# Performance work log

Measured on AMD Instinct MI355X. Metric: run time of the kernel, lower is better.

The kernel has to match this reference:

```python
import jax, jax.numpy as jnp
import numpy as np

DEPTH, DIM, HEADS = 12, 768, 12
B, N = 2, 2048
HEAD_DIM = DIM // HEADS


def setup_inputs() -> dict:
    key = jax.random.key(0)
    ks = jax.random.split(key, 8)
    s = 0.02
    return {
        "x": jax.random.normal(ks[0], (B, N, DIM), jnp.float32),
        "sequence_ids": jnp.sort(jax.random.randint(ks[1], (B, N), 0, 8), axis=-1),
        "sequence_mask": jnp.zeros((B, N), dtype=bool),
        "ln1_w": jnp.ones((DEPTH, DIM), jnp.float32),
        "ln1_b": jnp.zeros((DEPTH, DIM), jnp.float32),
        "qkv_w": jax.random.normal(ks[2], (DEPTH, DIM, 3 * DIM), jnp.float32) * s,
        "qkv_b": jnp.zeros((DEPTH, 3 * DIM), jnp.float32),
        "proj_w": jax.random.normal(ks[3], (DEPTH, DIM, DIM), jnp.float32) * s,
        "proj_b": jnp.zeros((DEPTH, DIM), jnp.float32),
        "ls1_g": jnp.full((DEPTH, DIM), 1e-5, jnp.float32),
        "ln2_w": jnp.ones((DEPTH, DIM), jnp.float32),
        "ln2_b": jnp.zeros((DEPTH, DIM), jnp.float32),
        "fc1_w": jax.random.normal(ks[4], (DEPTH, DIM, 4 * DIM), jnp.float32) * s,
        "fc1_b": jnp.zeros((DEPTH, 4 * DIM), jnp.float32),
        "fc2_w": jax.random.normal(ks[5], (DEPTH, 4 * DIM, DIM), jnp.float32) * s,
        "fc2_b": jnp.zeros((DEPTH, DIM), jnp.float32),
        "ls2_g": jnp.full((DEPTH, DIM), 1e-5, jnp.float32),
        "r": 0,
    }


def _layernorm(x, w, b, eps=1e-5):
    m = x.mean(-1, keepdims=True)
    v = ((x - m) ** 2).mean(-1, keepdims=True)
    return (x - m) * jax.lax.rsqrt(v + eps) * w + b


def _attention(x, attn_mask, qkv_w, qkv_b, proj_w, proj_b):
    b, n, c = x.shape
    qkv = (x @ qkv_w + qkv_b).reshape(b, n, 3, HEADS, HEAD_DIM)
    qkv = jnp.transpose(qkv, (2, 0, 3, 1, 4))  # [3, B, H, N, hd]
    q, k, v = qkv[0], qkv[1], qkv[2]
    attn = jnp.einsum("bhqd,bhkd->bhqk", q, k) * (HEAD_DIM ** -0.5)
    neg_inf = jnp.finfo(attn.dtype).min
    attn = jnp.where(attn_mask[:, None, :, :], neg_inf, attn)  # broadcast over heads
    attn = jax.nn.softmax(attn, axis=-1)
    out = jnp.einsum("bhqk,bhkd->bhqd", attn, v)
    out = jnp.transpose(out, (0, 2, 1, 3)).reshape(b, n, c)
    return out @ proj_w + proj_b


def reference(x, sequence_ids, sequence_mask, ln1_w, ln1_b, qkv_w, qkv_b,
              proj_w, proj_b, ls1_g, ln2_w, ln2_b, fc1_w, fc1_b,
              fc2_w, fc2_b, ls2_g, r):
    # attn_mask: True where attention is NOT allowed
    attn_mask = sequence_ids[:, :, None] != sequence_ids[:, None, :]
    attn_mask = attn_mask | sequence_mask[:, :, None] | sequence_mask[:, None, :]
    for i in range(DEPTH):
        h = _layernorm(x, ln1_w[i], ln1_b[i])
        h = _attention(h, attn_mask, qkv_w[i], qkv_b[i], proj_w[i], proj_b[i])
        x = x + h * ls1_g[i]
        h = _layernorm(x, ln2_w[i], ln2_b[i])
        h = jax.nn.gelu(h @ fc1_w[i] + fc1_b[i], approximate=False) @ fc2_w[i] + fc2_b[i]
        x = x + h * ls2_g[i]
    return x
```

## Files before the change

### kernel.cpp

```cpp
#include <hip/hip_runtime.h>

#define NDEPTH 12
#define NDIM 768
#define NHEADS 12
#define NB 2
#define NSEQ 2048
#define MTOK (NB*NSEQ)

typedef short bf16x8 __attribute__((ext_vector_type(8)));
typedef float f32x4 __attribute__((ext_vector_type(4)));
typedef unsigned short u16;
typedef unsigned int u32;

#define L2E 1.44269504088896f

__device__ inline u16 f2bf(float f){
  union { float f; u32 u; } x; x.f = f;
  u32 r = x.u + 0x7fffu + ((x.u >> 16) & 1u);
  return (u16)(r >> 16);
}

__device__ inline f32x4 mfma16(bf16x8 a, bf16x8 b, f32x4 c){
  return __builtin_amdgcn_mfma_f32_16x16x32_bf16(a, b, c, 0, 0, 0);
}

#define GLOAD_LDS(gsrc, ldst) __builtin_amdgcn_global_load_lds( \
    (const __attribute__((address_space(1))) u32*)(gsrc), \
    (__attribute__((address_space(3))) u32*)(ldst), 16, 0, 0)

__device__ inline void ln_body(const float* __restrict__ x,
    const float* __restrict__ w, const float* __restrict__ b,
    u16* __restrict__ out, int blk){
  int wv = threadIdx.x >> 6, lane = threadIdx.x & 63;
  int row = blk * 4 + wv;
  const float* xr = x + (size_t)row * NDIM;
  float v[12];
  #pragma unroll
  for (int j = 0; j < 12; j++) v[j] = xr[lane + 64*j];
  float s = 0.f;
  #pragma unroll
  for (int j = 0; j < 12; j++) s += v[j];
  #pragma unroll
  for (int m = 1; m < 64; m <<= 1) s += __shfl_xor(s, m);
  float mean = s * (1.0f/768.0f);
  float q = 0.f;
  #pragma unroll
  for (int j = 0; j < 12; j++){ float d = v[j]-mean; q += d*d; }
  #pragma unroll
  for (int m = 1; m < 64; m <<= 1) q += __shfl_xor(q, m);
  float rs = rsqrtf(q * (1.0f/768.0f) + 1e-5f);
  u16* orow = out + (size_t)row * NDIM;
  #pragma unroll
  for (int j = 0; j < 12; j++){
    int c = lane + 64*j;
    orow[c] = f2bf((v[j]-mean)*rs*w[c] + b[c]);
  }
}

__global__ __launch_bounds__(256) void ln_kernel(const float* __restrict__ x,
    const float* __restrict__ w, const float* __restrict__ b,
    u16* __restrict__ out){
  ln_body(x, w, b, out, blockIdx.x);
}

__device__ inline void wtrans_body(const float* __restrict__ in,
    u16* __restrict__ out, int K, int N, int n0, int k0, float* tile){
  int t = threadIdx.x;
  #pragma unroll
  for (int j = 0; j < 16; j++){
    int idx = t + j*256;
    int r = idx >> 6, c = idx & 63;
    tile[r*65 + c] = in[(size_t)(k0+r)*N + n0 + c];
  }
  __syncthreads();
  #pragma unroll
  for (int j = 0; j < 16; j++){
    int idx = t + j*256;
    int c = idx >> 6, r = idx & 63;
    out[(size_t)(n0+c)*K + k0 + r] = f2bf(tile[r*65 + c]);
  }
}

__global__ __launch_bounds__(256) void lnwt_kernel(
    const float* __restrict__ x, const float* __restrict__ lw,
    const float* __restrict__ lb, u16* __restrict__ lout,
    const float* __restrict__ qkvw, const float* __restrict__ projw,
    const float* __restrict__ fc1w, const float* __restrict__ fc2w,
    u16* __restrict__ wq, u16* __restrict__ wp,
    u16* __restrict__ w1, u16* __restrict__ w2){
  __shared__ float tile[64*65];
  int bid = blockIdx.x;
  if (bid < 1024){ ln_body(x, lw, lb, lout, bid); return; }
  bid -= 1024;
  const float* in; u16* out; int K, N, tl;
  if (bid < 432){        in = qkvw; out = wq; K = 768;  N = 2304; tl = bid; }
  else if (bid < 576){   in = projw; out = wp; K = 768; N = 768;  tl = bid - 432; }
  else if (bid < 1152){  in = fc1w; out = w1; K = 768;  N = 3072; tl = bid - 576; }
  else {                 in = fc2w; out = w2; K = 3072; N = 768;  tl = bid - 1152; }
  int ntn = N >> 6;
  int n0 = (tl % ntn) << 6, k0 = (tl / ntn) << 6;
  wtrans_body(in, out, K, N, n0, k0, tile);
}

__global__ __launch_bounds__(256) void wtrans12_kernel(
    const float* __restrict__ qkvw, const float* __restrict__ projw,
    const float* __restrict__ fc1w, const float* __restrict__ fc2w,
    u16* __restrict__ wbase){
  __shared__ float tile[64*65];
  int bid = blockIdx.x;
  int layer = bid / 1728, sub = bid % 1728;
  u16* wl = wbase + (size_t)layer * 7077888;
  const float* in; u16* out; int K, N, tl;
  if (sub < 432){       in = qkvw + (size_t)layer*768*2304; out = wl;                 K = 768;  N = 2304; tl = sub; }
  else if (sub < 576){  in = projw + (size_t)layer*768*768; out = wl + 1769472;       K = 768;  N = 768;  tl = sub - 432; }
  else if (sub < 1152){ in = fc1w + (size_t)layer*768*3072; out = wl + 2359296;       K = 768;  N = 3072; tl = sub - 576; }
  else {                in = fc2w + (size_t)layer*3072*768; out = wl + 4718592;       K = 3072; N = 768;  tl = sub - 1152; }
  int ntn = N >> 6;
  int n0 = (tl % ntn) << 6, k0 = (tl / ntn) << 6;
  wtrans_body(in, out, K, N, n0, k0, tile);
}

template<int BN, int EPI>
__global__ __launch_bounds__(512) void gemm_kernel(
    const u16* __restrict__ A, const u16* __restrict__ Wt,
    const float* __restrict__ bias, const float* __restrict__ g,
    u16* __restrict__ outb, float* __restrict__ xres,
    int M, int N, int K)
{
  constexpr int WGN = BN / 32;
  constexpr int WGM = 8 / WGN;
  constexpr int WTM = 128 / WGM;
  constexpr int MI = WTM / 16;
  constexpr int NI = 2;
  __shared__ u16 As[2][128*64];
  __shared__ u16 Bs[2][BN*64];
  int nwg = gridDim.x;
  int bid = (blockIdx.x & 7) * (nwg >> 3) + (blockIdx.x >> 3);
  int nt = N / BN;
  int bm = bid / nt, bn = bid % nt;
  int m0 = bm*128, n0 = bn*BN;
  int t = threadIdx.x, lane = t & 63, wv = t >> 6;
  int wm = (wv / WGN) * WTM, wn = (wv % WGN) * 32;
  f32x4 acc[MI][NI] = {};
  int fr = lane & 15, fg = lane >> 4;

  auto stage = [&](int bf, int k0){
    #pragma unroll
    for (int i = 0; i < 2; i++){
      int off = t*16 + i*8192;
      int row = off >> 7, cb = off & 127;
      const char* src = (const char*)A + ((size_t)(m0+row)*K + k0)*2 + (cb ^ ((row&7)<<4));
      GLOAD_LDS(src, (char*)As[bf] + off);
    }
    #pragma unroll
    for (int i = 0; i < BN/64; i++){
      int off = t*16 + i*8192;
      int row = off >> 7, cb = off & 127;
      const char* src = (const char*)Wt + ((size_t)(n0+row)*K + k0)*2 + (cb ^ ((row&7)<<4));
      GLOAD_LDS(src, (char*)Bs[bf] + off);
    }
  };

  stage(0, 0);
  stage(1, 64);
  int cur = 0;
  int NS = K >> 6;
  for (int i = 0; i < NS; i++){
    if constexpr (BN == 128) asm volatile("s_waitcnt vmcnt(4)" ::: "memory");
    else                     asm volatile("s_waitcnt vmcnt(3)" ::: "memory");
    asm volatile("s_barrier" ::: "memory");

    bf16x8 af[MI][2], bfv[NI][2];
    #pragma unroll
    for (int mi = 0; mi < MI; mi++)
      #pragma unroll
      for (int kh = 0; kh < 2; kh++){
        int row = wm + mi*16 + fr;
        int off = (row*128 + kh*64 + fg*16) ^ ((row&7)<<4);
        af[mi][kh] = *(const bf16x8*)((const char*)As[cur] + off);
      }
    #pragma unroll
    for (int ni = 0; ni < NI; ni++)
      #pragma unroll
      for (int kh = 0; kh < 2; kh++){
        int row = wn + ni*16 + fr;
        int off = (row*128 + kh*64 + fg*16) ^ ((row&7)<<4);
        bfv[ni][kh] = *(const bf16x8*)((const char*)Bs[cur] + off);
      }
    #pragma unroll
    for (int mi = 0; mi < MI; mi++)
      #pragma unroll
      for (int ni = 0; ni < NI; ni++){
        acc[mi][ni] = mfma16(af[mi][0], bfv[ni][0], acc[mi][ni]);
        acc[mi][ni] = mfma16(af[mi][1], bfv[ni][1], acc[mi][ni]);
      }

    asm volatile("s_barrier" ::: "memory");
    if (i + 2 < NS) stage(cur, (i + 2) << 6);
    cur ^= 1;
  }

  int fq = fg << 2;
  #pragma unroll
  for (int mi = 0; mi < MI; mi++){
    #pragma unroll
    for (int ni = 0; ni < NI; ni++){
      int col = n0 + wn + ni*16 + fr;
      float bv = bias[col];
      #pragma unroll
      for (int r = 0; r < 4; r++){
        int row = m0 + wm + mi*16 + fq + r;
        float v = acc[mi][ni][r] + bv;
        if (EPI == 0){
          outb[(size_t)row * N + col] = f2bf(v);
        } else if (EPI == 1){
          float ge = 0.5f * v * (1.0f + erff(v * 0.70710678118f));
          outb[(size_t)row * N + col] = f2bf(ge);
        } else {
          xres[(size_t)row * N + col] += v * g[col];
        }
      }
    }
  }
}

__global__ __launch_bounds__(256) void attn_kernel(
    const u16* __restrict__ qkv, const int* __restrict__ sid,
    const unsigned char* __restrict__ smask, u16* __restrict__ outb)
{
  __shared__ u16 Ks[64][72];
  __shared__ u16 Vs[64][72];
  __shared__ u16 Ps[4][16][72];
  int nwg = gridDim.x;
  int blk = (blockIdx.x & 7) * (nwg >> 3) + (blockIdx.x >> 3);
  int qt = blk & 31; int bh = blk >> 5;
  int b = bh / NHEADS, h = bh % NHEADS;
  int t = threadIdx.x, lane = t & 63, wv = t >> 6;
  int q0 = qt << 6;
  size_t rowbase = (size_t)b * NSEQ;
  int fr = lane & 15, fg8 = (lane >> 4) << 3, fq = (lane >> 4) << 2;

  int qrow = q0 + (wv << 4) + fr;
  const u16* qp = qkv + (rowbase + qrow) * 2304 + h*64 + fg8;
  bf16x8 qf0 = *(const bf16x8*)qp;
  bf16x8 qf1 = *(const bf16x8*)(qp + 32);

  int qlo = sid[rowbase + q0];
  int qhi = sid[rowbase + q0 + 63];

  int sq[4]; int mq[4];
  #pragma unroll
  for (int r = 0; r < 4; r++){
    int qr = q0 + (wv << 4) + fq + r;
    sq[r] = sid[rowbase + qr];
    mq[r] = smask[rowbase + qr];
  }
  float m[4], l[4]; f32x4 o[4] = {};
  #pragma unroll
  for (int r = 0; r < 4; r++){ m[r] = -3.0e38f; l[r] = 0.f; }

  int skk = t >> 2, sd = (t & 3) << 4;

  for (int kt = 0; kt < NSEQ/64; kt++){
    int klo = sid[rowbase + (kt << 6)];
    int khi = sid[rowbase + (kt << 6) + 63];
    if (khi < qlo || klo > qhi) continue;

    __syncthreads();
    int krow = (kt << 6) + skk;
    const u16* kp = qkv + (rowbase + krow) * 2304 + 768 + h*64 + sd;
    *(uint4*)&Ks[skk][sd]     = *(const uint4*)kp;
    *(uint4*)&Ks[skk][sd + 8] = *(const uint4*)(kp + 8);
    const u16* vp = kp + 768;
    uint4 v0 = *(const uint4*)vp, v1 = *(const uint4*)(vp + 8);
    {
      const u16* vv = (const u16*)&v0;
      #pragma unroll
      for (int i = 0; i < 8; i++) Vs[sd + i][skk] = vv[i];
      vv = (const u16*)&v1;
      #pragma unroll
      for (int i = 0; i < 8; i++) Vs[sd + 8 + i][skk] = vv[i];
    }
    int ks[4]; int mk[4];
    #pragma unroll
    for (int s2 = 0; s2 < 4; s2++){
      int kk = (kt << 6) + (s2 << 4) + fr;
      ks[s2] = sid[rowbase + kk];
      mk[s2] = smask[rowbase + kk];
    }
    __syncthreads();

    f32x4 S[4];
    #pragma unroll
    for (int s2 = 0; s2 < 4; s2++){
      bf16x8 kf0 = *(const bf16x8*)&Ks[(s2 << 4) + fr][fg8];
      bf16x8 kf1 = *(const bf16x8*)&Ks[(s2 << 4) + fr][fg8 + 32];
      f32x4 s = {};
      s = mfma16(qf0, kf0, s);
      s = mfma16(qf1, kf1, s);
      #pragma unroll
      for (int r = 0; r < 4; r++){
        float v = s[r] * 0.125f;
        bool msk = (mq[r] | mk[s2]) || (sq[r] != ks[s2]);
        S[s2][r] = msk ? -3.0e38f : v;
      }
    }
    float mn[4], sf[4], rs[4];
    #pragma unroll
    for (int r = 0; r < 4; r++){
      float mx = fmaxf(fmaxf(S[0][r], S[1][r]), fmaxf(S[2][r], S[3][r]));
      #pragma unroll
      for (int d = 1; d < 16; d <<= 1) mx = fmaxf(mx, __shfl_xor(mx, d));
      mn[r] = fmaxf(m[r], mx);
      sf[r] = exp2f((m[r] - mn[r]) * L2E);
      rs[r] = 0.f;
    }
    #pragma unroll
    for (int s2 = 0; s2 < 4; s2++){
      #pragma unroll
      for (int r = 0; r < 4; r++){
        float p = exp2f((S[s2][r] - mn[r]) * L2E);
        rs[r] += p;
        Ps[wv][fq + r][(s2 << 4) + fr] = f2bf(p);
      }
    }
    #pragma unroll
    for (int r = 0; r < 4; r++){
      #pragma unroll
      for (int d = 1; d < 16; d <<= 1) rs[r] += __shfl_xor(rs[r], d);
      l[r] = l[r] * sf[r] + rs[r];
      m[r] = mn[r];
    }
    #pragma unroll
    for (int dsub = 0; dsub < 4; dsub++)
      #pragma unroll
      for (int r = 0; r < 4; r++) o[dsub][r] *= sf[r];
    __syncthreads();
    #pragma unroll
    for (int kg = 0; kg < 2; kg++){
      bf16x8 pf = *(const bf16x8*)&Ps[wv][fr][(kg << 5) + fg8];
      #pragma unroll
      for (int dsub = 0; dsub < 4; dsub++){
        bf16x8 vf = *(const bf16x8*)&Vs[(dsub << 4) + fr][(kg << 5) + fg8];
        o[dsub] = mfma16(pf, vf, o[dsub]);
      }
    }
  }

  #pragma unroll
  for (int dsub = 0; dsub < 4; dsub++){
    #pragma unroll
    for (int r = 0; r < 4; r++){
      int row = q0 + (wv << 4) + fq + r;
      int col = h*64 + (dsub << 4) + fr;
      outb[(rowbase + row) * NDIM + col] = f2bf(o[dsub][r] / l[r]);
    }
  }
}

extern "C" void kernel_launch(void* const* d_in, const int* in_sizes, int n_in,
                              void* d_out, int out_size, void* d_ws, size_t ws_size,
                              hipStream_t stream) {
  const float* x_in = (const float*)d_in[0];
  const int* sid = (const int*)d_in[1];
  const unsigned char* smask = (const unsigned char*)d_in[2];
  const float* ln1w = (const float*)d_in[3];
  const float* ln1b = (const float*)d_in[4];
  const float* qkvw = (const float*)d_in[5];
  const float* qkvb = (const float*)d_in[6];
  const float* projw = (const float*)d_in[7];
  const float* projb = (const float*)d_in[8];
  const float* ls1 = (const float*)d_in[9];
  const float* ln2w = (const float*)d_in[10];
  const float* ln2b = (const float*)d_in[11];
  const float* fc1w = (const float*)d_in[12];
  const float* fc1b = (const float*)d_in[13];
  const float* fc2w = (const float*)d_in[14];
  const float* fc2b = (const float*)d_in[15];
  const float* ls2 = (const float*)d_in[16];

  float* x = (float*)d_out;
  char* ws = (char*)d_ws;
  u16* hbuf   = (u16*)ws;
  u16* qkvbuf = (u16*)(ws + (size_t)6291456);
  u16* abuf   = (u16*)(ws + (size_t)25165824);
  u16* mbuf   = (u16*)(ws + (size_t)31457280);
  const size_t WT0 = 56623104;

  bool upfront  = ws_size >= (size_t)226492416;
  bool fused_wt = !upfront && ws_size >= WT0 + (size_t)14155776;
  u16* wall = (u16*)(ws + WT0);

  hipMemcpyAsync(x, x_in, (size_t)MTOK*NDIM*4, hipMemcpyDeviceToDevice, stream);

  if (upfront)
    wtrans12_kernel<<<12*1728, 256, 0, stream>>>(qkvw, projw, fc1w, fc2w, wall);

  for (int i = 0; i < NDEPTH; i++){
    const float* qw = qkvw + (size_t)i*NDIM*2304;
    const float* pw = projw + (size_t)i*NDIM*NDIM;
    const float* f1 = fc1w + (size_t)i*NDIM*3072;
    const float* f2 = fc2w + (size_t)i*3072*NDIM;

    u16 *wq, *wp, *w1, *w2;
    if (upfront){
      wq = wall + (size_t)i*7077888;
      wp = wq + 1769472; w1 = wp + 589824; w2 = w1 + 2359296;
    } else if (fused_wt){
      wq = wall; wp = wq + (size_t)2304*768;
      w1 = wp + (size_t)768*768; w2 = w1 + (size_t)768*3072;
    } else {
      wq = wp = w1 = w2 = wall;
    }

    if (fused_wt){
      lnwt_kernel<<<2752, 256, 0, stream>>>(x, ln1w + i*NDIM, ln1b + i*NDIM, hbuf,
                                            qw, pw, f1, f2, wq, wp, w1, w2);
    } else {
      ln_kernel<<<MTOK/4, 256, 0, stream>>>(x, ln1w + i*NDIM, ln1b + i*NDIM, hbuf);
    }
    gemm_kernel<128,0><<<(MTOK/128)*(2304/128), 512, 0, stream>>>(
        hbuf, wq, qkvb + (size_t)i*2304, nullptr, qkvbuf, nullptr, MTOK, 2304, NDIM);
    attn_kernel<<<NB*NHEADS*(NSEQ/64), 256, 0, stream>>>(qkvbuf, sid, smask, abuf);
    gemm_kernel<64,2><<<(MTOK/128)*(NDIM/64), 512, 0, stream>>>(
        abuf, wp, projb + (size_t)i*NDIM, ls1 + (size_t)i*NDIM,
        nullptr, x, MTOK, NDIM, NDIM);
    ln_kernel<<<MTOK/4, 256, 0, stream>>>(x, ln2w + i*NDIM, ln2b + i*NDIM, hbuf);
    gemm_kernel<128,1><<<(MTOK/128)*(3072/128), 512, 0, stream>>>(
        hbuf, w1, fc1b + (size_t)i*3072, nullptr, mbuf, nullptr, MTOK, 3072, NDIM);
    gemm_kernel<64,2><<<(MTOK/128)*(NDIM/64), 512, 0, stream>>>(
        mbuf, w2, fc2b + (size_t)i*NDIM, ls2 + (size_t)i*NDIM,
        nullptr, x, MTOK, NDIM, 3072);
  }
}
```

Measured before the change: 2.193 ms.

## Vectorize layernorm and weight-transpose accesses; simplify GEMM prefetch to single-stage lookahead

Layernorm now reads rows as float4 and writes bf16 output in 4-element chunks. The weight transpose reads float4 and writes 8 bf16 values at once, replacing scalar accesses to cut memory transactions. The GEMM main loop drops the two-deep prefetch with explicit vmcnt waits and raw s_barrier. It now uses __syncthreads followed by a prefetch of only the next K-tile, which shortens the load lookahead and may expose more global-load latency in the dominant GEMMs. Host-side weight pointer selection is also reorganized.

```diff
diff --git a/kernel.cpp b/kernel.cpp
--- a/kernel.cpp
+++ b/kernel.cpp
@@ -36,7 +36,10 @@
   const float* xr = x + (size_t)row * NDIM;
   float v[12];
   #pragma unroll
-  for (int j = 0; j < 12; j++) v[j] = xr[lane + 64*j];
+  for (int j = 0; j < 3; j++){
+    float4 f = *(const float4*)&xr[4*lane + 256*j];
+    v[j*4+0] = f.x; v[j*4+1] = f.y; v[j*4+2] = f.z; v[j*4+3] = f.w;
+  }
   float s = 0.f;
   #pragma unroll
   for (int j = 0; j < 12; j++) s += v[j];
@@ -51,9 +54,13 @@
   float rs = rsqrtf(q * (1.0f/768.0f) + 1e-5f);
   u16* orow = out + (size_t)row * NDIM;
   #pragma unroll
-  for (int j = 0; j < 12; j++){
-    int c = lane + 64*j;
-    orow[c] = f2bf((v[j]-mean)*rs*w[c] + b[c]);
+  for (int j = 0; j < 3; j++){
+    int c0 = 4*lane + 256*j;
+    u16 tmp[4];
+    #pragma unroll
+    for (int i = 0; i < 4; i++)
+      tmp[i] = f2bf((v[j*4+i]-mean)*rs*w[c0+i] + b[c0+i]);
+    *(uint2*)&orow[c0] = *(uint2*)tmp;
   }
 }
 
@@ -67,17 +74,22 @@
     u16* __restrict__ out, int K, int N, int n0, int k0, float* tile){
   int t = threadIdx.x;
   #pragma unroll
-  for (int j = 0; j < 16; j++){
+  for (int j = 0; j < 4; j++){
     int idx = t + j*256;
-    int r = idx >> 6, c = idx & 63;
-    tile[r*65 + c] = in[(size_t)(k0+r)*N + n0 + c];
+    int r = idx >> 4, c4 = (idx & 15) << 2;
+    float4 f = *(const float4*)&in[(size_t)(k0+r)*N + n0 + c4];
+    float* tp = &tile[r*65 + c4];
+    tp[0] = f.x; tp[1] = f.y; tp[2] = f.z; tp[3] = f.w;
   }
   __syncthreads();
   #pragma unroll
-  for (int j = 0; j < 16; j++){
+  for (int j = 0; j < 2; j++){
     int idx = t + j*256;
-    int c = idx >> 6, r = idx & 63;
-    out[(size_t)(n0+c)*K + k0 + r] = f2bf(tile[r*65 + c]);
+    int c = idx >> 3, r8 = (idx & 7) << 3;
+    u16 tmp[8];
+    #pragma unroll
+    for (int i = 0; i < 8; i++) tmp[i] = f2bf(tile[(r8+i)*65 + c]);
+    *(uint4*)&out[(size_t)(n0+c)*K + k0 + r8] = *(uint4*)tmp;
   }
 }
 
@@ -162,13 +174,10 @@
   };
 
   stage(0, 0);
-  stage(1, 64);
   int cur = 0;
-  int NS = K >> 6;
-  for (int i = 0; i < NS; i++){
-    if constexpr (BN == 128) asm volatile("s_waitcnt vmcnt(4)" ::: "memory");
-    else                     asm volatile("s_waitcnt vmcnt(3)" ::: "memory");
-    asm volatile("s_barrier" ::: "memory");
+  for (int k0 = 0; k0 < K; k0 += 64){
+    __syncthreads();
+    if (k0 + 64 < K) stage(cur ^ 1, k0 + 64);
 
     bf16x8 af[MI][2], bfv[NI][2];
     #pragma unroll
@@ -194,9 +203,6 @@
         acc[mi][ni] = mfma16(af[mi][0], bfv[ni][0], acc[mi][ni]);
         acc[mi][ni] = mfma16(af[mi][1], bfv[ni][1], acc[mi][ni]);
       }
-
-    asm volatile("s_barrier" ::: "memory");
-    if (i + 2 < NS) stage(cur, (i + 2) << 6);
     cur ^= 1;
   }
 
@@ -406,14 +412,12 @@
     if (upfront){
       wq = wall + (size_t)i*7077888;
       wp = wq + 1769472; w1 = wp + 589824; w2 = w1 + 2359296;
-    } else if (fused_wt){
+    } else {
       wq = wall; wp = wq + (size_t)2304*768;
       w1 = wp + (size_t)768*768; w2 = w1 + (size_t)768*3072;
-    } else {
-      wq = wp = w1 = w2 = wall;
-    }
-
-    if (fused_wt){
+    }
+
+    if (!upfront && fused_wt){
       lnwt_kernel<<<2752, 256, 0, stream>>>(x, ln1w + i*NDIM, ln1b + i*NDIM, hbuf,
                                             qw, pw, f1, f2, wq, wp, w1, w2);
     } else {
```

New measurement: 2.257 ms. 2.9% more time.
